# Kernel optimization log

Measured on AMD Instinct MI355X. Metric: run time of the kernel, lower is better.

Reference implementation:

```python
import jax, jax.numpy as jnp
import numpy as np

B, C, H, W = 32, 256, 8, 8
N = H * W                      # n_objects = 64
D_G_IN = 2 * C + 2             # pair concat + 2-dim relative position = 514
HG = 512                       # g hidden / output dim
HF = 512                       # f hidden dim
D_OUT = 256                    # f output dim


def _relative_grid_feat():
    # feat[p, q, 0] = oh(p) - oh(q); feat[p, q, 1] = ow(p) - ow(q); zero-centered globally
    idx = jnp.arange(N)
    oh, ow = idx // W, idx % W
    r0 = (oh[:, None] - oh[None, :]).astype(jnp.float32)
    r1 = (ow[:, None] - ow[None, :]).astype(jnp.float32)
    rel = jnp.stack([r0, r1], axis=-1)  # [N, N, 2]
    return rel - rel.mean()


def setup_inputs() -> dict:
    key = jax.random.key(0)
    ks = jax.random.split(key, 11)
    s = 0.02
    return {
        "x": jax.random.normal(ks[0], (B, C, H, W), dtype=jnp.float32),
        "g_W0": jax.random.normal(ks[1], (D_G_IN, HG), dtype=jnp.float32) * s,
        "g_b0": jnp.zeros((HG,), dtype=jnp.float32),
        "g_W1": jax.random.normal(ks[2], (HG, HG), dtype=jnp.float32) * s,
        "g_b1": jnp.zeros((HG,), dtype=jnp.float32),
        "g_W2": jax.random.normal(ks[3], (HG, HG), dtype=jnp.float32) * s,
        "g_b2": jnp.zeros((HG,), dtype=jnp.float32),
        "f_W0": jax.random.normal(ks[4], (HG, HF), dtype=jnp.float32) * s,
        "f_b0": jnp.zeros((HF,), dtype=jnp.float32),
        "f_W1": jax.random.normal(ks[5], (HF, D_OUT), dtype=jnp.float32) * s,
        "f_b1": jnp.zeros((D_OUT,), dtype=jnp.float32),
    }


def reference(x, g_W0, g_b0, g_W1, g_b1, g_W2, g_b2, f_W0, f_b0, f_W1, f_b1):
    relu = jax.nn.relu
    x_flat = x.reshape(B, C, N)                     # [B, C, N]
    xT = jnp.transpose(x_flat, (0, 2, 1))           # [B, N, C]
    # pair index k = p*N + q: xi takes object q (inner), xj takes object p (outer)
    xi = jnp.broadcast_to(xT[:, None, :, :], (B, N, N, C))
    xj = jnp.broadcast_to(xT[:, :, None, :], (B, N, N, C))
    rel = jnp.broadcast_to(_relative_grid_feat()[None], (B, N, N, 2))
    pair = jnp.concatenate([xi, xj, rel], axis=-1)  # [B, N, N, 2C+2]
    # g MLP (nonlinear=True -> activation on output too)
    h = relu(jnp.einsum('bpqd,dh->bpqh', pair, g_W0) + g_b0)
    h = relu(jnp.einsum('bpqh,hk->bpqk', h, g_W1) + g_b1)
    relations = relu(jnp.einsum('bpqh,hk->bpqk', h, g_W2) + g_b2)  # [B, N, N, HG]
    embedding = relations.sum(axis=(1, 2))          # sum over all pairs -> [B, HG]
    # f MLP (linear output)
    hf = relu(embedding @ f_W0 + f_b0)
    out = hf @ f_W1 + f_b1                          # [B, D_OUT]
    return out
```

## Files before the change

kernel.cpp:

```cpp
#include <hip/hip_runtime.h>


typedef short short8 __attribute__((ext_vector_type(8)));
typedef float f32x16 __attribute__((ext_vector_type(16)));

__device__ __forceinline__ unsigned short f2bf(float f) {
    unsigned u = __builtin_bit_cast(unsigned, f);
    u = (u + 0x7FFFu + ((u >> 16) & 1u)) >> 16;
    return (unsigned short)u;
}

__device__ __forceinline__ unsigned cvt_pk(float a, float b) {
    unsigned r;
    asm("v_cvt_pk_bf16_f32 %0, %1, %2" : "=v"(r) : "v"(a), "v"(b));
    return r;
}

__global__ __launch_bounds__(512) void uv_kernel(
    const float* __restrict__ x, const float* __restrict__ W0,
    const float* __restrict__ b0, float* __restrict__ Up, float* __restrict__ Vp)
{
    __shared__ float xs[256 * 8];
    const int blk = blockIdx.x;
    const int b = blk >> 3, n0 = (blk & 7) * 8;
    const int tid = threadIdx.x;

    for (int i = tid; i < 2048; i += 512) {
        int c = i >> 3, r = i & 7;
        xs[i] = x[((size_t)b * 256 + c) * 64 + n0 + r];
    }
    __syncthreads();

    const int h = tid;
    float ua[8], va[8];
#pragma unroll
    for (int r = 0; r < 8; ++r) { ua[r] = 0.f; va[r] = 0.f; }

    for (int c = 0; c < 256; ++c) {
        float wa = W0[(size_t)c * 512 + h];
        float wb = W0[(size_t)(256 + c) * 512 + h];
#pragma unroll
        for (int r = 0; r < 8; ++r) {
            float xv = xs[c * 8 + r];
            ua[r] += xv * wa;
            va[r] += xv * wb;
        }
    }
    const float w2a = W0[(size_t)512 * 512 + h];
    const float w2b = W0[(size_t)513 * 512 + h];
    const float bb = b0[h];
#pragma unroll
    for (int r = 0; r < 8; ++r) {
        int n = n0 + r;
        float fh = (float)(n >> 3), fw = (float)(n & 7);
        Up[((size_t)b * 64 + n) * 512 + h] = ua[r] - fh * w2a - fw * w2b;
        Vp[((size_t)b * 64 + n) * 512 + h] = va[r] + fh * w2a + fw * w2b + bb;
    }
}

__global__ __launch_bounds__(256) void wswz_kernel(
    const float* __restrict__ W1, const float* __restrict__ W2,
    unsigned short* __restrict__ W1s, unsigned short* __restrict__ W2s)
{
    int gid = blockIdx.x * 256 + threadIdx.x;
    int m = gid >> 15;
    int idx = gid & 32767;
    int col = idx & 511;
    int kg = idx >> 9;
    const float* W = m ? W2 : W1;
    unsigned short* O = m ? W2s : W1s;
    short8 v;
#pragma unroll
    for (int j = 0; j < 8; ++j)
        v[j] = (short)f2bf(W[(size_t)(kg * 8 + j) * 512 + col]);
    *(short8*)(O + (size_t)idx * 8) = v;
}

__global__ __launch_bounds__(512, 4) void main_kernel(
    const float* __restrict__ Up, const float* __restrict__ Vp,
    const unsigned short* __restrict__ W1s, const unsigned short* __restrict__ W2s,
    const float* __restrict__ b1, const float* __restrict__ b2,
    float* __restrict__ partials)
{
    __shared__ __align__(16) unsigned char lds[64 * 1024];

    const int blk = blockIdx.x;
    const int b = blk >> 6, p = blk & 63;
    const int tid = threadIdx.x;
    const int lane = tid & 63, wave = tid >> 6;
    const int l31 = lane & 31, lg = lane >> 5;
    const int swz = (l31 & 15) << 4;
    const int wcol = wave * 64;

    {
        const int cc = tid & 63;
        const int r0 = tid >> 6;
        const float* vb = Vp + ((size_t)(b * 64 + p)) * 512 + cc * 8;
        float4 v0 = *(const float4*)(vb);
        float4 v1 = *(const float4*)(vb + 4);
#pragma unroll
        for (int it = 0; it < 8; ++it) {
            int row = r0 + it * 8;
            const float* ub = Up + ((size_t)(b * 64 + row)) * 512 + cc * 8;
            float4 u0 = *(const float4*)(ub);
            float4 u1 = *(const float4*)(ub + 4);
            uint4 w;
            w.x = cvt_pk(fmaxf(u0.x + v0.x, 0.f), fmaxf(u0.y + v0.y, 0.f));
            w.y = cvt_pk(fmaxf(u0.z + v0.z, 0.f), fmaxf(u0.w + v0.w, 0.f));
            w.z = cvt_pk(fmaxf(u1.x + v1.x, 0.f), fmaxf(u1.y + v1.y, 0.f));
            w.w = cvt_pk(fmaxf(u1.z + v1.z, 0.f), fmaxf(u1.w + v1.w, 0.f));
            int off = row * 1024 + ((cc * 16) ^ ((row & 15) << 4));
            *(uint4*)(&lds[off]) = w;
        }
    }
    __syncthreads();

    f32x16 acc[2][2];
#pragma unroll
    for (int i = 0; i < 2; ++i)
#pragma unroll
        for (int j = 0; j < 2; ++j) acc[i][j] = (f32x16)0.f;

    const int arow0 = l31 * 1024;
    const int arow1 = (l31 + 32) * 1024;

    __builtin_amdgcn_s_setprio(1);
#pragma unroll 2
    for (int ks = 0; ks < 32; ++ks) {
        int achunk = (ks * 32 + lg * 16) ^ swz;
        short8 h0q0 = *(const short8*)(&lds[arow0 + achunk]);
        short8 h0q1 = *(const short8*)(&lds[arow1 + achunk]);
        const unsigned short* bp = W1s + ((size_t)((ks * 2 + lg) * 512 + wcol + l31)) * 8;
        short8 wv0 = *(const short8*)(bp);
        short8 wv1 = *(const short8*)(bp + 32 * 8);
        acc[0][0] = __builtin_amdgcn_mfma_f32_32x32x16_bf16(wv0, h0q0, acc[0][0], 0, 0, 0);
        acc[1][0] = __builtin_amdgcn_mfma_f32_32x32x16_bf16(wv1, h0q0, acc[1][0], 0, 0, 0);
        acc[0][1] = __builtin_amdgcn_mfma_f32_32x32x16_bf16(wv0, h0q1, acc[0][1], 0, 0, 0);
        acc[1][1] = __builtin_amdgcn_mfma_f32_32x32x16_bf16(wv1, h0q1, acc[1][1], 0, 0, 0);
    }
    __builtin_amdgcn_s_setprio(0);
    __syncthreads();

    {
#pragma unroll
        for (int hf = 0; hf < 2; ++hf) {
#pragma unroll
            for (int g = 0; g < 4; ++g) {
                int h = wcol + hf * 32 + g * 8 + 4 * lg;
                float4 bb = *(const float4*)(b1 + h);
#pragma unroll
                for (int qf = 0; qf < 2; ++qf) {
                    int q = qf * 32 + l31;
                    float a0 = fmaxf(acc[hf][qf][g * 4 + 0] + bb.x, 0.f);
                    float a1 = fmaxf(acc[hf][qf][g * 4 + 1] + bb.y, 0.f);
                    float a2 = fmaxf(acc[hf][qf][g * 4 + 2] + bb.z, 0.f);
                    float a3 = fmaxf(acc[hf][qf][g * 4 + 3] + bb.w, 0.f);
                    uint2 pk;
                    pk.x = cvt_pk(a0, a1);
                    pk.y = cvt_pk(a2, a3);
                    int off = q * 1024 + ((h * 2) ^ ((q & 15) << 4));
                    *(uint2*)(&lds[off]) = pk;
                }
            }
        }
    }
    __syncthreads();

    f32x16 acc2[2][2];
#pragma unroll
    for (int i = 0; i < 2; ++i)
#pragma unroll
        for (int j = 0; j < 2; ++j) acc2[i][j] = (f32x16)0.f;

    __builtin_amdgcn_s_setprio(1);
#pragma unroll 2
    for (int ks = 0; ks < 32; ++ks) {
        int achunk = (ks * 32 + lg * 16) ^ swz;
        short8 a0 = *(const short8*)(&lds[arow0 + achunk]);
        short8 a1 = *(const short8*)(&lds[arow1 + achunk]);
        const unsigned short* bp = W2s + ((size_t)((ks * 2 + lg) * 512 + wcol + l31)) * 8;
        short8 bv0 = *(const short8*)(bp);
        short8 bv1 = *(const short8*)(bp + 32 * 8);
        acc2[0][0] = __builtin_amdgcn_mfma_f32_32x32x16_bf16(a0, bv0, acc2[0][0], 0, 0, 0);
        acc2[1][0] = __builtin_amdgcn_mfma_f32_32x32x16_bf16(a1, bv0, acc2[1][0], 0, 0, 0);
        acc2[0][1] = __builtin_amdgcn_mfma_f32_32x32x16_bf16(a0, bv1, acc2[0][1], 0, 0, 0);
        acc2[1][1] = __builtin_amdgcn_mfma_f32_32x32x16_bf16(a1, bv1, acc2[1][1], 0, 0, 0);
    }
    __builtin_amdgcn_s_setprio(0);

    {
        float s[2];
#pragma unroll
        for (int cf = 0; cf < 2; ++cf) {
            int col = wcol + cf * 32 + l31;
            float bias = b2[col];
            float t = 0.f;
#pragma unroll
            for (int rf = 0; rf < 2; ++rf)
#pragma unroll
                for (int reg = 0; reg < 16; ++reg)
                    t += fmaxf(acc2[rf][cf][reg] + bias, 0.f);
            t += __shfl_xor(t, 32);
            s[cf] = t;
        }
        if (lane < 32) {
            partials[(size_t)blk * 512 + wcol + lane] = s[0];
            partials[(size_t)blk * 512 + wcol + 32 + lane] = s[1];
        }
    }
}

__global__ __launch_bounds__(256) void reduce_f_kernel(
    const float* __restrict__ partials,
    const float* __restrict__ fW0, const float* __restrict__ fb0,
    const float* __restrict__ fW1, const float* __restrict__ fb1,
    float* __restrict__ out)
{
    __shared__ float es[512];
    __shared__ float hs[512];
    const int b = blockIdx.x, tid = threadIdx.x;

    float s0 = 0.f, s1 = 0.f;
    const float* base = partials + (size_t)b * 64 * 512;
#pragma unroll 8
    for (int p = 0; p < 64; ++p) {
        s0 += base[(size_t)p * 512 + tid];
        s1 += base[(size_t)p * 512 + tid + 256];
    }
    es[tid] = s0;
    es[tid + 256] = s1;
    __syncthreads();

    float a0 = fb0[tid], a1 = fb0[tid + 256];
    for (int c = 0; c < 512; ++c) {
        float e = es[c];
        a0 += e * fW0[(size_t)c * 512 + tid];
        a1 += e * fW0[(size_t)c * 512 + tid + 256];
    }
    hs[tid] = fmaxf(a0, 0.f);
    hs[tid + 256] = fmaxf(a1, 0.f);
    __syncthreads();

    float o = fb1[tid];
    for (int c = 0; c < 512; ++c) o += hs[c] * fW1[(size_t)c * 256 + tid];
    out[b * 256 + tid] = o;
}

extern "C" void kernel_launch(void* const* d_in, const int* in_sizes, int n_in,
                              void* d_out, int out_size, void* d_ws, size_t ws_size,
                              hipStream_t stream)
{
    const float* x   = (const float*)d_in[0];
    const float* gW0 = (const float*)d_in[1];
    const float* gb0 = (const float*)d_in[2];
    const float* gW1 = (const float*)d_in[3];
    const float* gb1 = (const float*)d_in[4];
    const float* gW2 = (const float*)d_in[5];
    const float* gb2 = (const float*)d_in[6];
    const float* fW0 = (const float*)d_in[7];
    const float* fb0 = (const float*)d_in[8];
    const float* fW1 = (const float*)d_in[9];
    const float* fb1 = (const float*)d_in[10];
    float* out = (float*)d_out;

    char* ws = (char*)d_ws;
    float* Up              = (float*)(ws);
    float* Vp              = (float*)(ws + (4  << 20));
    unsigned short* W1s    = (unsigned short*)(ws + (8 << 20));
    unsigned short* W2s    = (unsigned short*)(ws + (8 << 20) + (512 << 10));
    float* partials        = (float*)(ws + (9  << 20));

    uv_kernel<<<256, 512, 0, stream>>>(x, gW0, gb0, Up, Vp);
    wswz_kernel<<<256, 256, 0, stream>>>(gW1, gW2, W1s, W2s);
    main_kernel<<<2048, 512, 0, stream>>>(Up, Vp, W1s, W2s, gb1, gb2, partials);
    reduce_f_kernel<<<32, 256, 0, stream>>>(partials, fW0, fb0, fW1, fb1, out);
}
```

Baseline: 212.8 us.

## Process two outer objects per workgroup, atomically reduce embedding, split f MLP

Each main_kernel workgroup now handles two p rows, using 128KB of dynamic LDS, so every W1/W2 fragment loaded from global memory feeds twice as many MFMAs, and the grid is remapped across XCDs. The per-block partial sums are accumulated with float atomics into a zeroed embedding buffer instead of a separate reduction pass. The f MLP is split into two kernels with many more blocks to parallelize the small GEMVs. In exchange, occupancy drops to 2 blocks per CU with doubled accumulators, and atomic summation order becomes nondeterministic.

```diff
diff --git a/kernel.cpp b/kernel.cpp
--- a/kernel.cpp
+++ b/kernel.cpp
@@ -60,9 +60,11 @@
 
 __global__ __launch_bounds__(256) void wswz_kernel(
     const float* __restrict__ W1, const float* __restrict__ W2,
-    unsigned short* __restrict__ W1s, unsigned short* __restrict__ W2s)
+    unsigned short* __restrict__ W1s, unsigned short* __restrict__ W2s,
+    float* __restrict__ emb)
 {
     int gid = blockIdx.x * 256 + threadIdx.x;
+    if (gid < 16384) emb[gid] = 0.f;
     int m = gid >> 15;
     int idx = gid & 32767;
     int col = idx & 511;
@@ -76,16 +78,19 @@
     *(short8*)(O + (size_t)idx * 8) = v;
 }
 
-__global__ __launch_bounds__(512, 4) void main_kernel(
+__global__ __launch_bounds__(512, 2) void main_kernel(
     const float* __restrict__ Up, const float* __restrict__ Vp,
     const unsigned short* __restrict__ W1s, const unsigned short* __restrict__ W2s,
     const float* __restrict__ b1, const float* __restrict__ b2,
-    float* __restrict__ partials)
-{
-    __shared__ __align__(16) unsigned char lds[64 * 1024];
-
-    const int blk = blockIdx.x;
-    const int b = blk >> 6, p = blk & 63;
+    float* __restrict__ emb)
+{
+    extern __shared__ __align__(16) unsigned char lds[];
+    unsigned char* T[2] = { lds, lds + 65536 };
+
+    const int wg = ((blockIdx.x & 7) << 7) | (blockIdx.x >> 3);
+    const int b = wg >> 5, pp = wg & 31;
+    const int p0 = pp * 2, p1 = p0 + 1;
+
     const int tid = threadIdx.x;
     const int lane = tid & 63, wave = tid >> 6;
     const int l31 = lane & 31, lg = lane >> 5;
@@ -95,48 +100,62 @@
     {
         const int cc = tid & 63;
         const int r0 = tid >> 6;
-        const float* vb = Vp + ((size_t)(b * 64 + p)) * 512 + cc * 8;
-        float4 v0 = *(const float4*)(vb);
-        float4 v1 = *(const float4*)(vb + 4);
+        const float* vA = Vp + ((size_t)(b * 64 + p0)) * 512 + cc * 8;
+        const float* vB = Vp + ((size_t)(b * 64 + p1)) * 512 + cc * 8;
+        float4 vA0 = *(const float4*)(vA),     vA1 = *(const float4*)(vA + 4);
+        float4 vB0 = *(const float4*)(vB),     vB1 = *(const float4*)(vB + 4);
 #pragma unroll
         for (int it = 0; it < 8; ++it) {
             int row = r0 + it * 8;
             const float* ub = Up + ((size_t)(b * 64 + row)) * 512 + cc * 8;
             float4 u0 = *(const float4*)(ub);
             float4 u1 = *(const float4*)(ub + 4);
+            int off = row * 1024 + ((cc * 16) ^ ((row & 15) << 4));
             uint4 w;
-            w.x = cvt_pk(fmaxf(u0.x + v0.x, 0.f), fmaxf(u0.y + v0.y, 0.f));
-            w.y = cvt_pk(fmaxf(u0.z + v0.z, 0.f), fmaxf(u0.w + v0.w, 0.f));
-            w.z = cvt_pk(fmaxf(u1.x + v1.x, 0.f), fmaxf(u1.y + v1.y, 0.f));
-            w.w = cvt_pk(fmaxf(u1.z + v1.z, 0.f), fmaxf(u1.w + v1.w, 0.f));
-            int off = row * 1024 + ((cc * 16) ^ ((row & 15) << 4));
-            *(uint4*)(&lds[off]) = w;
-        }
-    }
-    __syncthreads();
-
-    f32x16 acc[2][2];
-#pragma unroll
-    for (int i = 0; i < 2; ++i)
-#pragma unroll
-        for (int j = 0; j < 2; ++j) acc[i][j] = (f32x16)0.f;
+            w.x = cvt_pk(fmaxf(u0.x + vA0.x, 0.f), fmaxf(u0.y + vA0.y, 0.f));
+            w.y = cvt_pk(fmaxf(u0.z + vA0.z, 0.f), fmaxf(u0.w + vA0.w, 0.f));
+            w.z = cvt_pk(fmaxf(u1.x + vA1.x, 0.f), fmaxf(u1.y + vA1.y, 0.f));
+            w.w = cvt_pk(fmaxf(u1.z + vA1.z, 0.f), fmaxf(u1.w + vA1.w, 0.f));
+            *(uint4*)(&T[0][off]) = w;
+            w.x = cvt_pk(fmaxf(u0.x + vB0.x, 0.f), fmaxf(u0.y + vB0.y, 0.f));
+            w.y = cvt_pk(fmaxf(u0.z + vB0.z, 0.f), fmaxf(u0.w + vB0.w, 0.f));
+            w.z = cvt_pk(fmaxf(u1.x + vB1.x, 0.f), fmaxf(u1.y + vB1.y, 0.f));
+            w.w = cvt_pk(fmaxf(u1.z + vB1.z, 0.f), fmaxf(u1.w + vB1.w, 0.f));
+            *(uint4*)(&T[1][off]) = w;
+        }
+    }
+    __syncthreads();
 
     const int arow0 = l31 * 1024;
     const int arow1 = (l31 + 32) * 1024;
+
+    f32x16 acc[2][2][2];
+#pragma unroll
+    for (int t = 0; t < 2; ++t)
+#pragma unroll
+        for (int i = 0; i < 2; ++i)
+#pragma unroll
+            for (int j = 0; j < 2; ++j) acc[t][i][j] = (f32x16)0.f;
 
     __builtin_amdgcn_s_setprio(1);
 #pragma unroll 2
     for (int ks = 0; ks < 32; ++ks) {
         int achunk = (ks * 32 + lg * 16) ^ swz;
-        short8 h0q0 = *(const short8*)(&lds[arow0 + achunk]);
-        short8 h0q1 = *(const short8*)(&lds[arow1 + achunk]);
+        short8 a00 = *(const short8*)(&T[0][arow0 + achunk]);
+        short8 a01 = *(const short8*)(&T[0][arow1 + achunk]);
+        short8 a10 = *(const short8*)(&T[1][arow0 + achunk]);
+        short8 a11 = *(const short8*)(&T[1][arow1 + achunk]);
         const unsigned short* bp = W1s + ((size_t)((ks * 2 + lg) * 512 + wcol + l31)) * 8;
         short8 wv0 = *(const short8*)(bp);
         short8 wv1 = *(const short8*)(bp + 32 * 8);
-        acc[0][0] = __builtin_amdgcn_mfma_f32_32x32x16_bf16(wv0, h0q0, acc[0][0], 0, 0, 0);
-        acc[1][0] = __builtin_amdgcn_mfma_f32_32x32x16_bf16(wv1, h0q0, acc[1][0], 0, 0, 0);
-        acc[0][1] = __builtin_amdgcn_mfma_f32_32x32x16_bf16(wv0, h0q1, acc[0][1], 0, 0, 0);
-        acc[1][1] = __builtin_amdgcn_mfma_f32_32x32x16_bf16(wv1, h0q1, acc[1][1], 0, 0, 0);
+        acc[0][0][0] = __builtin_amdgcn_mfma_f32_32x32x16_bf16(wv0, a00, acc[0][0][0], 0, 0, 0);
+        acc[0][1][0] = __builtin_amdgcn_mfma_f32_32x32x16_bf16(wv1, a00, acc[0][1][0], 0, 0, 0);
+        acc[0][0][1] = __builtin_amdgcn_mfma_f32_32x32x16_bf16(wv0, a01, acc[0][0][1], 0, 0, 0);
+        acc[0][1][1] = __builtin_amdgcn_mfma_f32_32x32x16_bf16(wv1, a01, acc[0][1][1], 0, 0, 0);
+        acc[1][0][0] = __builtin_amdgcn_mfma_f32_32x32x16_bf16(wv0, a10, acc[1][0][0], 0, 0, 0);
+        acc[1][1][0] = __builtin_amdgcn_mfma_f32_32x32x16_bf16(wv1, a10, acc[1][1][0], 0, 0, 0);
+        acc[1][0][1] = __builtin_amdgcn_mfma_f32_32x32x16_bf16(wv0, a11, acc[1][0][1], 0, 0, 0);
+        acc[1][1][1] = __builtin_amdgcn_mfma_f32_32x32x16_bf16(wv1, a11, acc[1][1][1], 0, 0, 0);
     }
     __builtin_amdgcn_s_setprio(0);
     __syncthreads();
@@ -149,42 +168,53 @@
                 int h = wcol + hf * 32 + g * 8 + 4 * lg;
                 float4 bb = *(const float4*)(b1 + h);
 #pragma unroll
-                for (int qf = 0; qf < 2; ++qf) {
-                    int q = qf * 32 + l31;
-                    float a0 = fmaxf(acc[hf][qf][g * 4 + 0] + bb.x, 0.f);
-                    float a1 = fmaxf(acc[hf][qf][g * 4 + 1] + bb.y, 0.f);
-                    float a2 = fmaxf(acc[hf][qf][g * 4 + 2] + bb.z, 0.f);
-                    float a3 = fmaxf(acc[hf][qf][g * 4 + 3] + bb.w, 0.f);
-                    uint2 pk;
-                    pk.x = cvt_pk(a0, a1);
-                    pk.y = cvt_pk(a2, a3);
-                    int off = q * 1024 + ((h * 2) ^ ((q & 15) << 4));
-                    *(uint2*)(&lds[off]) = pk;
+                for (int t = 0; t < 2; ++t) {
+#pragma unroll
+                    for (int qf = 0; qf < 2; ++qf) {
+                        int q = qf * 32 + l31;
+                        float a0 = fmaxf(acc[t][hf][qf][g * 4 + 0] + bb.x, 0.f);
+                        float a1 = fmaxf(acc[t][hf][qf][g * 4 + 1] + bb.y, 0.f);
+                        float a2 = fmaxf(acc[t][hf][qf][g * 4 + 2] + bb.z, 0.f);
+                        float a3 = fmaxf(acc[t][hf][qf][g * 4 + 3] + bb.w, 0.f);
+                        uint2 pk;
+                        pk.x = cvt_pk(a0, a1);
+                        pk.y = cvt_pk(a2, a3);
+                        int off = q * 1024 + ((h * 2) ^ ((q & 15) << 4));
+                        *(uint2*)(&T[t][off]) = pk;
+                    }
                 }
             }
         }
     }
     __syncthreads();
 
-    f32x16 acc2[2][2];
-#pragma unroll
-    for (int i = 0; i < 2; ++i)
-#pragma unroll
-        for (int j = 0; j < 2; ++j) acc2[i][j] = (f32x16)0.f;
+    f32x16 acc2[2][2][2];
+#pragma unroll
+    for (int t = 0; t < 2; ++t)
+#pragma unroll
+        for (int i = 0; i < 2; ++i)
+#pragma unroll
+            for (int j = 0; j < 2; ++j) acc2[t][i][j] = (f32x16)0.f;
 
     __builtin_amdgcn_s_setprio(1);
 #pragma unroll 2
     for (int ks = 0; ks < 32; ++ks) {
         int achunk = (ks * 32 + lg * 16) ^ swz;
-        short8 a0 = *(const short8*)(&lds[arow0 + achunk]);
-        short8 a1 = *(const short8*)(&lds[arow1 + achunk]);
+        short8 a00 = *(const short8*)(&T[0][arow0 + achunk]);
+        short8 a01 = *(const short8*)(&T[0][arow1 + achunk]);
+        short8 a10 = *(const short8*)(&T[1][arow0 + achunk]);
+        short8 a11 = *(const short8*)(&T[1][arow1 + achunk]);
         const unsigned short* bp = W2s + ((size_t)((ks * 2 + lg) * 512 + wcol + l31)) * 8;
         short8 bv0 = *(const short8*)(bp);
         short8 bv1 = *(const short8*)(bp + 32 * 8);
-        acc2[0][0] = __builtin_amdgcn_mfma_f32_32x32x16_bf16(a0, bv0, acc2[0][0], 0, 0, 0);
-        acc2[1][0] = __builtin_amdgcn_mfma_f32_32x32x16_bf16(a1, bv0, acc2[1][0], 0, 0, 0);
-        acc2[0][1] = __builtin_amdgcn_mfma_f32_32x32x16_bf16(a0, bv1, acc2[0][1], 0, 0, 0);
-        acc2[1][1] = __builtin_amdgcn_mfma_f32_32x32x16_bf16(a1, bv1, acc2[1][1], 0, 0, 0);
+        acc2[0][0][0] = __builtin_amdgcn_mfma_f32_32x32x16_bf16(a00, bv0, acc2[0][0][0], 0, 0, 0);
+        acc2[0][1][0] = __builtin_amdgcn_mfma_f32_32x32x16_bf16(a01, bv0, acc2[0][1][0], 0, 0, 0);
+        acc2[0][0][1] = __builtin_amdgcn_mfma_f32_32x32x16_bf16(a00, bv1, acc2[0][0][1], 0, 0, 0);
+        acc2[0][1][1] = __builtin_amdgcn_mfma_f32_32x32x16_bf16(a01, bv1, acc2[0][1][1], 0, 0, 0);
+        acc2[1][0][0] = __builtin_amdgcn_mfma_f32_32x32x16_bf16(a10, bv0, acc2[1][0][0], 0, 0, 0);
+        acc2[1][1][0] = __builtin_amdgcn_mfma_f32_32x32x16_bf16(a11, bv0, acc2[1][1][0], 0, 0, 0);
+        acc2[1][0][1] = __builtin_amdgcn_mfma_f32_32x32x16_bf16(a10, bv1, acc2[1][0][1], 0, 0, 0);
+        acc2[1][1][1] = __builtin_amdgcn_mfma_f32_32x32x16_bf16(a11, bv1, acc2[1][1][1], 0, 0, 0);
     }
     __builtin_amdgcn_s_setprio(0);
 
@@ -194,56 +224,73 @@
         for (int cf = 0; cf < 2; ++cf) {
             int col = wcol + cf * 32 + l31;
             float bias = b2[col];
-            float t = 0.f;
-#pragma unroll
-            for (int rf = 0; rf < 2; ++rf)
-#pragma unroll
-                for (int reg = 0; reg < 16; ++reg)
-                    t += fmaxf(acc2[rf][cf][reg] + bias, 0.f);
-            t += __shfl_xor(t, 32);
-            s[cf] = t;
+            float tt = 0.f;
+#pragma unroll
+            for (int t = 0; t < 2; ++t)
+#pragma unroll
+                for (int rf = 0; rf < 2; ++rf)
+#pragma unroll
+                    for (int reg = 0; reg < 16; ++reg)
+                        tt += fmaxf(acc2[t][rf][cf][reg] + bias, 0.f);
+            tt += __shfl_xor(tt, 32);
+            s[cf] = tt;
         }
         if (lane < 32) {
-            partials[(size_t)blk * 512 + wcol + lane] = s[0];
-            partials[(size_t)blk * 512 + wcol + 32 + lane] = s[1];
-        }
-    }
-}
-
-__global__ __launch_bounds__(256) void reduce_f_kernel(
-    const float* __restrict__ partials,
-    const float* __restrict__ fW0, const float* __restrict__ fb0,
-    const float* __restrict__ fW1, const float* __restrict__ fb1,
-    float* __restrict__ out)
+            unsafeAtomicAdd(&emb[b * 512 + wcol + lane], s[0]);
+            unsafeAtomicAdd(&emb[b * 512 + wcol + 32 + lane], s[1]);
+        }
+    }
+}
+
+__global__ __launch_bounds__(256) void f0_kernel(
+    const float* __restrict__ emb, const float* __restrict__ fW0,
+    const float* __restrict__ fb0, float* __restrict__ hs)
 {
     __shared__ float es[512];
-    __shared__ float hs[512];
-    const int b = blockIdx.x, tid = threadIdx.x;
-
-    float s0 = 0.f, s1 = 0.f;
-    const float* base = partials + (size_t)b * 64 * 512;
-#pragma unroll 8
-    for (int p = 0; p < 64; ++p) {
-        s0 += base[(size_t)p * 512 + tid];
-        s1 += base[(size_t)p * 512 + tid + 256];
-    }
-    es[tid] = s0;
-    es[tid + 256] = s1;
-    __syncthreads();
-
-    float a0 = fb0[tid], a1 = fb0[tid + 256];
-    for (int c = 0; c < 512; ++c) {
-        float e = es[c];
-        a0 += e * fW0[(size_t)c * 512 + tid];
-        a1 += e * fW0[(size_t)c * 512 + tid + 256];
-    }
-    hs[tid] = fmaxf(a0, 0.f);
-    hs[tid + 256] = fmaxf(a1, 0.f);
-    __syncthreads();
-
-    float o = fb1[tid];
-    for (int c = 0; c < 512; ++c) o += hs[c] * fW1[(size_t)c * 256 + tid];
-    out[b * 256 + tid] = o;
+    __shared__ float red[256];
+    const int b = blockIdx.x >> 3, s = blockIdx.x & 7;
+    const int t = threadIdx.x;
+    const int colL = t & 63, cg = t >> 6;
+    es[t] = emb[b * 512 + t];
+    es[t + 256] = emb[b * 512 + 256 + t];
+    __syncthreads();
+    const int col = s * 64 + colL;
+    float a = 0.f;
+    const int c0 = cg * 128;
+#pragma unroll 4
+    for (int c = c0; c < c0 + 128; ++c)
+        a += es[c] * fW0[(size_t)c * 512 + col];
+    red[t] = a;
+    __syncthreads();
+    if (t < 64) {
+        float r = red[t] + red[t + 64] + red[t + 128] + red[t + 192] + fb0[col];
+        hs[b * 512 + col] = fmaxf(r, 0.f);
+    }
+}
+
+__global__ __launch_bounds__(256) void f1_kernel(
+    const float* __restrict__ hs, const float* __restrict__ fW1,
+    const float* __restrict__ fb1, float* __restrict__ out)
+{
+    __shared__ float es[512];
+    __shared__ float red[256];
+    const int b = blockIdx.x >> 2, s = blockIdx.x & 3;
+    const int t = threadIdx.x;
+    const int colL = t & 63, cg = t >> 6;
+    es[t] = hs[b * 512 + t];
+    es[t + 256] = hs[b * 512 + 256 + t];
+    __syncthreads();
+    const int col = s * 64 + colL;
+    float a = 0.f;
+    const int c0 = cg * 128;
+#pragma unroll 4
+    for (int c = c0; c < c0 + 128; ++c)
+        a += es[c] * fW1[(size_t)c * 256 + col];
+    red[t] = a;
+    __syncthreads();
+    if (t < 64) {
+        out[b * 256 + col] = red[t] + red[t + 64] + red[t + 128] + red[t + 192] + fb1[col];
+    }
 }
 
 extern "C" void kernel_launch(void* const* d_in, const int* in_sizes, int n_in,
@@ -264,14 +311,16 @@
     float* out = (float*)d_out;
 
     char* ws = (char*)d_ws;
-    float* Up              = (float*)(ws);
-    float* Vp              = (float*)(ws + (4  << 20));
-    unsigned short* W1s    = (unsigned short*)(ws + (8 << 20));
-    unsigned short* W2s    = (unsigned short*)(ws + (8 << 20) + (512 << 10));
-    float* partials        = (float*)(ws + (9  << 20));
+    float* Up           = (float*)(ws);
+    float* Vp           = (float*)(ws + (4 << 20));
+    unsigned short* W1s = (unsigned short*)(ws + (8 << 20));
+    unsigned short* W2s = (unsigned short*)(ws + (8 << 20) + (512 << 10));
+    float* emb          = (float*)(ws + (9 << 20));
+    float* hs           = (float*)(ws + (9 << 20) + (64 << 10));
 
     uv_kernel<<<256, 512, 0, stream>>>(x, gW0, gb0, Up, Vp);
-    wswz_kernel<<<256, 256, 0, stream>>>(gW1, gW2, W1s, W2s);
-    main_kernel<<<2048, 512, 0, stream>>>(Up, Vp, W1s, W2s, gb1, gb2, partials);
-    reduce_f_kernel<<<32, 256, 0, stream>>>(partials, fW0, fb0, fW1, fb1, out);
-}
+    wswz_kernel<<<256, 256, 0, stream>>>(gW1, gW2, W1s, W2s, emb);
+    main_kernel<<<1024, 512, 131072, stream>>>(Up, Vp, W1s, W2s, gb1, gb2, emb);
+    f0_kernel<<<256, 256, 0, stream>>>(emb, fW0, fb0, hs);
+    f1_kernel<<<128, 256, 0, stream>>>(hs, fW1, fb1, out);
+}
```

After: 177.8 us. -16.4%, faster.
